# Kernel tuning notes

Hardware: AMD Instinct MI355X
Metric: run time of the kernel (lower is better)

## Reference

```python
import jax, jax.numpy as jnp
import numpy as np
import math

B, T, C, H, E = 1, 384, 512, 8, 16
D = C // H

def layer_norm(x, w, b, eps=1e-5):
    mu = jnp.mean(x, axis=-1, keepdims=True)
    var = jnp.mean(jnp.square(x - mu), axis=-1, keepdims=True)
    return (x - mu) * jax.lax.rsqrt(var + eps) * w + b

def setup_inputs() -> dict:
    key = jax.random.key(0)
    ks = jax.random.split(key, 12)
    s = 0.02
    return {
        'x': jax.random.normal(ks[0], (B, T, C), jnp.float32),
        'bias_matrix': jax.random.randint(ks[1], (B, T, T), 0, E, jnp.int32),
        'ln1_w': jnp.ones((C,), jnp.float32),
        'ln1_b': jnp.zeros((C,), jnp.float32),
        'w_attn_w': jax.random.normal(ks[2], (3 * C, C), jnp.float32) * s,
        'w_attn_b': jnp.zeros((3 * C,), jnp.float32),
        'w_proj_w': jax.random.normal(ks[3], (C, C), jnp.float32) * s,
        'w_proj_b': jnp.zeros((C,), jnp.float32),
        'attn_bias_emb': jax.random.normal(ks[4], (E, H), jnp.float32) * s,
        'edge_emb': jax.random.normal(ks[5], (E, C), jnp.float32) * s,
        'w_edge_k_w': jax.random.normal(ks[6], (C, C), jnp.float32) * s,
        'w_edge_k_b': jnp.zeros((C,), jnp.float32),
        'w_edge_v_w': jax.random.normal(ks[7], (C, C), jnp.float32) * s,
        'w_edge_v_b': jnp.zeros((C,), jnp.float32),
        'ln2_w': jnp.ones((C,), jnp.float32),
        'ln2_b': jnp.zeros((C,), jnp.float32),
        'c_fc_w': jax.random.normal(ks[8], (4 * C, C), jnp.float32) * s,
        'c_fc_b': jnp.zeros((4 * C,), jnp.float32),
        'c_proj_w': jax.random.normal(ks[9], (C, 4 * C), jnp.float32) * s,
        'c_proj_b': jnp.zeros((C,), jnp.float32),
    }

def reference(x, bias_matrix, ln1_w, ln1_b, w_attn_w, w_attn_b, w_proj_w, w_proj_b,
              attn_bias_emb, edge_emb, w_edge_k_w, w_edge_k_b, w_edge_v_w, w_edge_v_b,
              ln2_w, ln2_b, c_fc_w, c_fc_b, c_proj_w, c_proj_b):
    # --- attention branch ---
    h = layer_norm(x, ln1_w, ln1_b)
    qkv = h @ w_attn_w.T + w_attn_b                      # (B,T,3C)
    q, k, v = jnp.split(qkv, 3, axis=-1)
    q = q.reshape(B, T, H, D).transpose(0, 2, 1, 3)      # (B,H,T,D)
    k = k.reshape(B, T, H, D).transpose(0, 2, 1, 3)
    v = v.reshape(B, T, H, D).transpose(0, 2, 1, 3)
    scale = math.sqrt(D)

    ee = edge_emb[bias_matrix]                           # (B,T,T,C)
    e_k = (ee @ w_edge_k_w.T + w_edge_k_b).reshape(B, T, T, H, D)
    # score[b,h,i,j] = sum_d q[b,h,i,d] * k[b,h,j,d] * e_k[b,i,j,h,d]
    scores = jnp.einsum('bhid,bhjd,bijhd->bhij', q, k, e_k) / scale

    mask = jnp.tril(jnp.ones((T, T), bool))              # causal, diag included
    scores = jnp.where(mask, scores, -jnp.inf)
    ab = attn_bias_emb[bias_matrix].transpose(0, 3, 1, 2)  # (B,H,T,T)
    ab = jnp.where(mask, ab, 0.0)
    attn = jax.nn.softmax(scores + ab, axis=-1)

    e_v = (ee @ w_edge_v_w.T + w_edge_v_b).reshape(B, T, T, H, D)
    # y[b,h,i,d] = sum_j attn[b,h,i,j] * v[b,h,j,d] * e_v[b,i,j,h,d]
    y = jnp.einsum('bhij,bhjd,bijhd->bhid', attn, v, e_v)
    y = y.transpose(0, 2, 1, 3).reshape(B, T, C)
    y = y @ w_proj_w.T + w_proj_b
    x = x + y

    # --- MLP branch ---
    h2 = layer_norm(x, ln2_w, ln2_b)
    h2 = jax.nn.gelu(h2 @ c_fc_w.T + c_fc_b, approximate=False)
    x = x + (h2 @ c_proj_w.T + c_proj_b)
    return x
```

## Files before the change

kernel.cpp:

```cpp
#include <hip/hip_runtime.h>
#include <math.h>

#define TT 384
#define CC 512
#define HH 8
#define EE 16

typedef __bf16 bf16_t;
typedef __bf16 bf16x8 __attribute__((ext_vector_type(8)));
typedef __bf16 bf16x4v __attribute__((ext_vector_type(4)));
typedef float f32x4 __attribute__((ext_vector_type(4)));

__device__ __forceinline__ float wave_reduce_sum(float v) {
#pragma unroll
  for (int off = 32; off >= 1; off >>= 1) v += __shfl_xor(v, off, 64);
  return v;
}
__device__ __forceinline__ float wave_reduce_max(float v) {
#pragma unroll
  for (int off = 32; off >= 1; off >>= 1) v = fmaxf(v, __shfl_xor(v, off, 64));
  return v;
}

__global__ __launch_bounds__(256) void pre_k(
    const float* __restrict__ x, const float* __restrict__ ln1_w,
    const float* __restrict__ ln1_b, bf16_t* __restrict__ hbuf,
    const float* __restrict__ edge_emb, const float* __restrict__ wk,
    const float* __restrict__ kb, const float* __restrict__ wv,
    const float* __restrict__ vb, float* __restrict__ ek_tab,
    float* __restrict__ ev_tab) {
  __shared__ float sh[8];
  int tid = threadIdx.x;
  if (blockIdx.x < 384) {
    int row = blockIdx.x;
    const float* xr = x + (size_t)row * CC;
    float v0 = xr[tid], v1 = xr[tid + 256];
    float s = wave_reduce_sum(v0 + v1);
    float q = wave_reduce_sum(v0 * v0 + v1 * v1);
    int wv_ = tid >> 6, ln_ = tid & 63;
    if (ln_ == 0) { sh[wv_] = s; sh[4 + wv_] = q; }
    __syncthreads();
    float stot = sh[0] + sh[1] + sh[2] + sh[3];
    float qtot = sh[4] + sh[5] + sh[6] + sh[7];
    float mu = stot * (1.0f / 512.0f);
    float var = qtot * (1.0f / 512.0f) - mu * mu;
    float rs = rsqrtf(var + 1e-5f);
    hbuf[(size_t)row * CC + tid] =
        (bf16_t)((v0 - mu) * rs * ln1_w[tid] + ln1_b[tid]);
    hbuf[(size_t)row * CC + tid + 256] =
        (bf16_t)((v1 - mu) * rs * ln1_w[tid + 256] + ln1_b[tid + 256]);
  } else {
    int wid = (blockIdx.x - 384) * 4 + (tid >> 6);
    int lane = tid & 63;
    int gbase = wid * 16;
    int table = gbase >> 13;
    int e = (gbase >> 9) & 15;
    int c0 = gbase & 511;
    const float* er = edge_emb + e * 512 + lane * 8;
    f32x4 ea = *(const f32x4*)er;
    f32x4 eb = *(const f32x4*)(er + 4);
    const float* wbase = table ? wv : wk;
    const float* bbase = table ? vb : kb;
    float* obase = (table ? ev_tab : ek_tab) + e * 512;
#pragma unroll
    for (int o = 0; o < 16; o++) {
      int c = c0 + o;
      const float* wr = wbase + (size_t)c * 512 + lane * 8;
      f32x4 wa = *(const f32x4*)wr;
      f32x4 wb = *(const f32x4*)(wr + 4);
      float acc = ea.x * wa.x + ea.y * wa.y + ea.z * wa.z + ea.w * wa.w +
                  eb.x * wb.x + eb.y * wb.y + eb.z * wb.z + eb.w * wb.w;
      acc = wave_reduce_sum(acc);
      if (lane == 0) obase[c] = acc + bbase[c];
    }
  }
}

__global__ void ln_k(const float* __restrict__ xin, const float* __restrict__ w,
                     const float* __restrict__ b, bf16_t* __restrict__ out) {
  __shared__ float sh[8];
  int row = blockIdx.x, tid = threadIdx.x;
  const float* xr = xin + (size_t)row * CC;
  float v0 = xr[tid], v1 = xr[tid + 256];
  float s = wave_reduce_sum(v0 + v1);
  float q = wave_reduce_sum(v0 * v0 + v1 * v1);
  int wv_ = tid >> 6, ln_ = tid & 63;
  if (ln_ == 0) { sh[wv_] = s; sh[4 + wv_] = q; }
  __syncthreads();
  float stot = sh[0] + sh[1] + sh[2] + sh[3];
  float qtot = sh[4] + sh[5] + sh[6] + sh[7];
  float mu = stot * (1.0f / 512.0f);
  float var = qtot * (1.0f / 512.0f) - mu * mu;
  float rs = rsqrtf(var + 1e-5f);
  out[(size_t)row * CC + tid] = (bf16_t)((v0 - mu) * rs * w[tid] + b[tid]);
  out[(size_t)row * CC + tid + 256] =
      (bf16_t)((v1 - mu) * rs * w[tid + 256] + b[tid + 256]);
}

__device__ __forceinline__ bf16x8 load_w_frag(const float* p) {
  f32x4 a = *(const f32x4*)p;
  f32x4 b = *(const f32x4*)(p + 4);
  bf16x8 r;
  r[0] = (bf16_t)a.x; r[1] = (bf16_t)a.y; r[2] = (bf16_t)a.z; r[3] = (bf16_t)a.w;
  r[4] = (bf16_t)b.x; r[5] = (bf16_t)b.y; r[6] = (bf16_t)b.z; r[7] = (bf16_t)b.w;
  return r;
}

template <int MODE>
__global__ __launch_bounds__(256) void gemm_sk(
    const bf16_t* __restrict__ A, const float* __restrict__ W,
    const float* __restrict__ bias, const float* __restrict__ res,
    void* __restrict__ out, int N, int K) {
  __shared__ float part[4][32][32];
  int tid = threadIdx.x;
  int lane = tid & 63, wave = tid >> 6;
  int m0 = blockIdx.y * 32, n0 = blockIdx.x * 32;
  int r16 = lane & 15, quad = lane >> 4;
  int kchunk = K >> 2;
  int k0 = wave * kchunk;

  f32x4 acc[2][2];
  f32x4 zero = {0.f, 0.f, 0.f, 0.f};
#pragma unroll
  for (int i = 0; i < 2; i++)
#pragma unroll
    for (int j = 0; j < 2; j++) acc[i][j] = zero;

  const bf16_t* Ap = A + (size_t)(m0 + r16) * K + k0 + quad * 8;
  const float* Wp = W + (size_t)(n0 + r16) * K + k0 + quad * 8;
  for (int kb = 0; kb < kchunk; kb += 32) {
    bf16x8 af[2], bfr[2];
#pragma unroll
    for (int t = 0; t < 2; t++)
      af[t] = *(const bf16x8*)(Ap + (size_t)t * 16 * K + kb);
#pragma unroll
    for (int t = 0; t < 2; t++)
      bfr[t] = load_w_frag(Wp + (size_t)t * 16 * K + kb);
#pragma unroll
    for (int i = 0; i < 2; i++)
#pragma unroll
      for (int j = 0; j < 2; j++)
        acc[i][j] = __builtin_amdgcn_mfma_f32_16x16x32_bf16(af[i], bfr[j],
                                                            acc[i][j], 0, 0, 0);
  }

#pragma unroll
  for (int i = 0; i < 2; i++)
#pragma unroll
    for (int j = 0; j < 2; j++)
#pragma unroll
      for (int r = 0; r < 4; r++)
        part[wave][i * 16 + quad * 4 + r][j * 16 + r16] = acc[i][j][r];
  __syncthreads();

  int row = tid >> 3, c4 = (tid & 7) * 4;
  f32x4 v = *(const f32x4*)&part[0][row][c4];
  v += *(const f32x4*)&part[1][row][c4];
  v += *(const f32x4*)&part[2][row][c4];
  v += *(const f32x4*)&part[3][row][c4];
  int grow = m0 + row, gcol = n0 + c4;
  v += *(const f32x4*)(bias + gcol);
  if (MODE == 1) {
#pragma unroll
    for (int t = 0; t < 4; t++)
      v[t] = 0.5f * v[t] * (1.0f + erff(v[t] * 0.70710678118654752f));
  }
  if (MODE == 2 || MODE == 3) {
    v += *(const f32x4*)(res + (size_t)grow * N + gcol);
    *(f32x4*)((float*)out + (size_t)grow * N + gcol) = v;
  } else {
    bf16x4v o;
#pragma unroll
    for (int t = 0; t < 4; t++) o[t] = (bf16_t)v[t];
    *(bf16x4v*)((bf16_t*)out + (size_t)grow * N + gcol) = o;
  }
}

__global__ __launch_bounds__(256) void attn_k(
    const bf16_t* __restrict__ qkv, const int* __restrict__ bias_matrix,
    const float* __restrict__ attn_bias_emb, const float* __restrict__ ek_tab,
    const float* __restrict__ ev_tab, bf16_t* __restrict__ ybuf) {
  __shared__ float s[TT];
  __shared__ int ebuf[TT];
  __shared__ float qe[EE][68];
  __shared__ float evh[EE * 64];
  __shared__ float red[4 * 64];
  __shared__ float absh[EE];
  __shared__ float scr[8];

  int i = blockIdx.x, h = blockIdx.y;
  int tid = threadIdx.x, lane = tid & 63, wave = tid >> 6;
  int n = i + 1;

  for (int j = tid; j < n; j += 256) ebuf[j] = bias_matrix[i * TT + j];
  if (tid < EE) absh[tid] = attn_bias_emb[tid * HH + h];
  for (int idx = tid; idx < EE * 64; idx += 256) {
    int e = idx >> 6, d = idx & 63;
    float qv = (float)qkv[(size_t)i * 1536 + h * 64 + d];
    qe[e][d] = qv * ek_tab[e * 512 + h * 64 + d];
    evh[idx] = ev_tab[e * 512 + h * 64 + d];
  }
  __syncthreads();

  for (int jl = tid; jl < n; jl += 256) {
    int e = ebuf[jl];
    const uint4* kp = (const uint4*)(qkv + (size_t)jl * 1536 + 512 + h * 64);
    uint4 kr[8];
#pragma unroll
    for (int dg = 0; dg < 8; dg++) kr[dg] = kp[dg];
    float acc = 0.f;
#pragma unroll
    for (int dg = 0; dg < 8; dg++) {
      bf16x8 kv = *reinterpret_cast<const bf16x8*>(&kr[dg]);
      f32x4 qa = *(const f32x4*)&qe[e][dg * 8];
      f32x4 qb = *(const f32x4*)&qe[e][dg * 8 + 4];
      acc += (float)kv[0] * qa.x + (float)kv[1] * qa.y +
             (float)kv[2] * qa.z + (float)kv[3] * qa.w +
             (float)kv[4] * qb.x + (float)kv[5] * qb.y +
             (float)kv[6] * qb.z + (float)kv[7] * qb.w;
    }
    s[jl] = acc * 0.125f + absh[e];
  }
  __syncthreads();

  float lm = -1e30f;
  for (int j = tid; j < n; j += 256) lm = fmaxf(lm, s[j]);
  lm = wave_reduce_max(lm);
  if (lane == 0) scr[wave] = lm;
  __syncthreads();
  float mx = fmaxf(fmaxf(scr[0], scr[1]), fmaxf(scr[2], scr[3]));
  float ls = 0.0f;
  for (int j = tid; j < n; j += 256) {
    float p = __expf(s[j] - mx);
    s[j] = p;
    ls += p;
  }
  ls = wave_reduce_sum(ls);
  if (lane == 0) scr[4 + wave] = ls;
  __syncthreads();
  float inv = 1.0f / (scr[4] + scr[5] + scr[6] + scr[7]);

  float acc = 0.0f;
  int j = wave;
  for (; j + 4 < n; j += 8) {
    int e0 = ebuf[j], e1 = ebuf[j + 4];
    float p0 = s[j], p1 = s[j + 4];
    float v0 = (float)qkv[(size_t)j * 1536 + 1024 + h * 64 + lane];
    float v1 = (float)qkv[(size_t)(j + 4) * 1536 + 1024 + h * 64 + lane];
    acc += p0 * v0 * evh[e0 * 64 + lane] + p1 * v1 * evh[e1 * 64 + lane];
  }
  for (; j < n; j += 4) {
    int e = ebuf[j];
    float vv = (float)qkv[(size_t)j * 1536 + 1024 + h * 64 + lane];
    acc += s[j] * vv * evh[e * 64 + lane];
  }
  red[wave * 64 + lane] = acc;
  __syncthreads();
  if (tid < 64) {
    float y = (red[tid] + red[64 + tid] + red[128 + tid] + red[192 + tid]) * inv;
    ybuf[(size_t)i * CC + h * 64 + tid] = (bf16_t)y;
  }
}

extern "C" void kernel_launch(void* const* d_in, const int* in_sizes, int n_in,
                              void* d_out, int out_size, void* d_ws,
                              size_t ws_size, hipStream_t stream) {
  const float* x = (const float*)d_in[0];
  const int* bias_mat = (const int*)d_in[1];
  const float* ln1_w = (const float*)d_in[2];
  const float* ln1_b = (const float*)d_in[3];
  const float* w_attn_w = (const float*)d_in[4];
  const float* w_attn_b = (const float*)d_in[5];
  const float* w_proj_w = (const float*)d_in[6];
  const float* w_proj_b = (const float*)d_in[7];
  const float* attn_bias_emb = (const float*)d_in[8];
  const float* edge_emb = (const float*)d_in[9];
  const float* w_edge_k_w = (const float*)d_in[10];
  const float* w_edge_k_b = (const float*)d_in[11];
  const float* w_edge_v_w = (const float*)d_in[12];
  const float* w_edge_v_b = (const float*)d_in[13];
  const float* ln2_w = (const float*)d_in[14];
  const float* ln2_b = (const float*)d_in[15];
  const float* c_fc_w = (const float*)d_in[16];
  const float* c_fc_b = (const float*)d_in[17];
  const float* c_proj_w = (const float*)d_in[18];
  const float* c_proj_b = (const float*)d_in[19];

  char* wp = (char*)d_ws;
  float* ek_tab = (float*)wp;   wp += 16 * 512 * 4;
  float* ev_tab = (float*)wp;   wp += 16 * 512 * 4;
  bf16_t* hbuf = (bf16_t*)wp;   wp += 384 * 512 * 2;
  bf16_t* qkv = (bf16_t*)wp;    wp += 384 * 1536 * 2;
  bf16_t* ybuf = (bf16_t*)wp;   wp += 384 * 512 * 2;
  float* x1 = (float*)wp;       wp += 384 * 512 * 4;
  bf16_t* h2 = (bf16_t*)wp;     wp += 384 * 512 * 2;
  bf16_t* gbuf = (bf16_t*)wp;   wp += 384 * 2048 * 2;

  pre_k<<<640, 256, 0, stream>>>(x, ln1_w, ln1_b, hbuf, edge_emb, w_edge_k_w,
                                 w_edge_k_b, w_edge_v_w, w_edge_v_b, ek_tab,
                                 ev_tab);
  gemm_sk<0><<<dim3(48, 12), 256, 0, stream>>>(hbuf, w_attn_w, w_attn_b,
                                               nullptr, qkv, 1536, 512);
  attn_k<<<dim3(TT, HH), 256, 0, stream>>>(qkv, bias_mat, attn_bias_emb,
                                           ek_tab, ev_tab, ybuf);
  gemm_sk<2><<<dim3(16, 12), 256, 0, stream>>>(ybuf, w_proj_w, w_proj_b, x, x1,
                                               512, 512);
  ln_k<<<384, 256, 0, stream>>>(x1, ln2_w, ln2_b, h2);
  gemm_sk<1><<<dim3(64, 12), 256, 0, stream>>>(h2, c_fc_w, c_fc_b, nullptr,
                                               gbuf, 2048, 512);
  gemm_sk<3><<<dim3(16, 12), 256, 0, stream>>>(gbuf, c_proj_w, c_proj_b, x1,
                                               (float*)d_out, 512, 2048);
}
```

Baseline: 182.6 us.

## Fuse all stages into one persistent kernel with grid barriers

Replaces the seven kernel launches with one persistent kernel of 512 blocks. The stages are separated by atomic-counter grid barriers, and a shared-memory union is reused across stages. All weights are converted to bf16 once in the first phase, so the GEMM inner loops load bf16 directly. Attention work is paired as row p with row 383-p to balance the causal load. This is meant to remove launch gaps and the fp32-to-bf16 conversion in the GEMM loops, at the cost of spin-wait barriers, a memset launch and a deadlock risk if not all blocks are co-resident.

```diff
diff --git a/kernel.cpp b/kernel.cpp
--- a/kernel.cpp
+++ b/kernel.cpp
@@ -5,12 +5,31 @@
 #define CC 512
 #define HH 8
 #define EE 16
+#define GRID 512
 
 typedef __bf16 bf16_t;
 typedef __bf16 bf16x8 __attribute__((ext_vector_type(8)));
 typedef __bf16 bf16x4v __attribute__((ext_vector_type(4)));
 typedef float f32x4 __attribute__((ext_vector_type(4)));
 
+struct Args {
+  const float* x; const int* bm;
+  const float *ln1w, *ln1b, *wattnb, *wprojb, *abemb, *eemb;
+  const float *wekw, *wekb, *wevw, *wevb, *ln2w, *ln2b, *cfcb, *cprojb;
+  const float *wattn, *wproj, *cfcw, *cprojw;
+  float *ektab, *evtab, *x1, *out;
+  bf16_t *hbuf, *qkv, *ybuf, *h2, *gbuf;
+  bf16_t *wattn_bf, *wproj_bf, *cfc_bf, *cproj_bf;
+  unsigned* bar;
+};
+
+struct SharedG { float part[4][32][32]; };
+struct SharedA {
+  float s[TT]; int ebuf[TT]; float qe[EE][68]; float evh[EE * 64];
+  float red[256]; float absh[EE]; float scr[8];
+};
+union SharedU { SharedG g; SharedA a; float sh[8]; };
+
 __device__ __forceinline__ float wave_reduce_sum(float v) {
 #pragma unroll
   for (int off = 32; off >= 1; off >>= 1) v += __shfl_xor(v, off, 64);
@@ -22,73 +41,33 @@
   return v;
 }
 
-__global__ __launch_bounds__(256) void pre_k(
-    const float* __restrict__ x, const float* __restrict__ ln1_w,
-    const float* __restrict__ ln1_b, bf16_t* __restrict__ hbuf,
-    const float* __restrict__ edge_emb, const float* __restrict__ wk,
-    const float* __restrict__ kb, const float* __restrict__ wv,
-    const float* __restrict__ vb, float* __restrict__ ek_tab,
-    float* __restrict__ ev_tab) {
-  __shared__ float sh[8];
+__device__ __forceinline__ void gbar(unsigned* c) {
+  __syncthreads();
+  if (threadIdx.x == 0) {
+    __threadfence();
+    __hip_atomic_fetch_add(c, 1u, __ATOMIC_ACQ_REL, __HIP_MEMORY_SCOPE_AGENT);
+    while (__hip_atomic_load(c, __ATOMIC_ACQUIRE, __HIP_MEMORY_SCOPE_AGENT) <
+           (unsigned)GRID)
+      __builtin_amdgcn_s_sleep(2);
+    __threadfence();
+  }
+  __syncthreads();
+}
+
+__device__ void ln_row(const float* __restrict__ xin, const float* __restrict__ w,
+                       const float* __restrict__ b, bf16_t* __restrict__ out,
+                       int row, SharedU& su) {
   int tid = threadIdx.x;
-  if (blockIdx.x < 384) {
-    int row = blockIdx.x;
-    const float* xr = x + (size_t)row * CC;
-    float v0 = xr[tid], v1 = xr[tid + 256];
-    float s = wave_reduce_sum(v0 + v1);
-    float q = wave_reduce_sum(v0 * v0 + v1 * v1);
-    int wv_ = tid >> 6, ln_ = tid & 63;
-    if (ln_ == 0) { sh[wv_] = s; sh[4 + wv_] = q; }
-    __syncthreads();
-    float stot = sh[0] + sh[1] + sh[2] + sh[3];
-    float qtot = sh[4] + sh[5] + sh[6] + sh[7];
-    float mu = stot * (1.0f / 512.0f);
-    float var = qtot * (1.0f / 512.0f) - mu * mu;
-    float rs = rsqrtf(var + 1e-5f);
-    hbuf[(size_t)row * CC + tid] =
-        (bf16_t)((v0 - mu) * rs * ln1_w[tid] + ln1_b[tid]);
-    hbuf[(size_t)row * CC + tid + 256] =
-        (bf16_t)((v1 - mu) * rs * ln1_w[tid + 256] + ln1_b[tid + 256]);
-  } else {
-    int wid = (blockIdx.x - 384) * 4 + (tid >> 6);
-    int lane = tid & 63;
-    int gbase = wid * 16;
-    int table = gbase >> 13;
-    int e = (gbase >> 9) & 15;
-    int c0 = gbase & 511;
-    const float* er = edge_emb + e * 512 + lane * 8;
-    f32x4 ea = *(const f32x4*)er;
-    f32x4 eb = *(const f32x4*)(er + 4);
-    const float* wbase = table ? wv : wk;
-    const float* bbase = table ? vb : kb;
-    float* obase = (table ? ev_tab : ek_tab) + e * 512;
-#pragma unroll
-    for (int o = 0; o < 16; o++) {
-      int c = c0 + o;
-      const float* wr = wbase + (size_t)c * 512 + lane * 8;
-      f32x4 wa = *(const f32x4*)wr;
-      f32x4 wb = *(const f32x4*)(wr + 4);
-      float acc = ea.x * wa.x + ea.y * wa.y + ea.z * wa.z + ea.w * wa.w +
-                  eb.x * wb.x + eb.y * wb.y + eb.z * wb.z + eb.w * wb.w;
-      acc = wave_reduce_sum(acc);
-      if (lane == 0) obase[c] = acc + bbase[c];
-    }
-  }
-}
-
-__global__ void ln_k(const float* __restrict__ xin, const float* __restrict__ w,
-                     const float* __restrict__ b, bf16_t* __restrict__ out) {
-  __shared__ float sh[8];
-  int row = blockIdx.x, tid = threadIdx.x;
+  __syncthreads();
   const float* xr = xin + (size_t)row * CC;
   float v0 = xr[tid], v1 = xr[tid + 256];
   float s = wave_reduce_sum(v0 + v1);
   float q = wave_reduce_sum(v0 * v0 + v1 * v1);
   int wv_ = tid >> 6, ln_ = tid & 63;
-  if (ln_ == 0) { sh[wv_] = s; sh[4 + wv_] = q; }
-  __syncthreads();
-  float stot = sh[0] + sh[1] + sh[2] + sh[3];
-  float qtot = sh[4] + sh[5] + sh[6] + sh[7];
+  if (ln_ == 0) { su.sh[wv_] = s; su.sh[4 + wv_] = q; }
+  __syncthreads();
+  float stot = su.sh[0] + su.sh[1] + su.sh[2] + su.sh[3];
+  float qtot = su.sh[4] + su.sh[5] + su.sh[6] + su.sh[7];
   float mu = stot * (1.0f / 512.0f);
   float var = qtot * (1.0f / 512.0f) - mu * mu;
   float rs = rsqrtf(var + 1e-5f);
@@ -97,27 +76,41 @@
       (bf16_t)((v1 - mu) * rs * w[tid + 256] + b[tid + 256]);
 }
 
-__device__ __forceinline__ bf16x8 load_w_frag(const float* p) {
-  f32x4 a = *(const f32x4*)p;
-  f32x4 b = *(const f32x4*)(p + 4);
-  bf16x8 r;
-  r[0] = (bf16_t)a.x; r[1] = (bf16_t)a.y; r[2] = (bf16_t)a.z; r[3] = (bf16_t)a.w;
-  r[4] = (bf16_t)b.x; r[5] = (bf16_t)b.y; r[6] = (bf16_t)b.z; r[7] = (bf16_t)b.w;
-  return r;
+__device__ void table_unit(int idx, const Args& A) {
+  int tid = threadIdx.x, lane = tid & 63;
+  int wid = idx * 4 + (tid >> 6);
+  int gbase = wid * 16;
+  int table = gbase >> 13;
+  int e = (gbase >> 9) & 15;
+  int c0 = gbase & 511;
+  const float* er = A.eemb + e * 512 + lane * 8;
+  f32x4 ea = *(const f32x4*)er;
+  f32x4 eb = *(const f32x4*)(er + 4);
+  const float* wbase = table ? A.wevw : A.wekw;
+  const float* bbase = table ? A.wevb : A.wekb;
+  float* obase = (table ? A.evtab : A.ektab) + e * 512;
+#pragma unroll
+  for (int o = 0; o < 16; o++) {
+    int c = c0 + o;
+    const float* wr = wbase + (size_t)c * 512 + lane * 8;
+    f32x4 wa = *(const f32x4*)wr;
+    f32x4 wb = *(const f32x4*)(wr + 4);
+    float acc = ea.x * wa.x + ea.y * wa.y + ea.z * wa.z + ea.w * wa.w +
+                eb.x * wb.x + eb.y * wb.y + eb.z * wb.z + eb.w * wb.w;
+    acc = wave_reduce_sum(acc);
+    if (lane == 0) obase[c] = acc + bbase[c];
+  }
 }
 
 template <int MODE>
-__global__ __launch_bounds__(256) void gemm_sk(
-    const bf16_t* __restrict__ A, const float* __restrict__ W,
-    const float* __restrict__ bias, const float* __restrict__ res,
-    void* __restrict__ out, int N, int K) {
-  __shared__ float part[4][32][32];
-  int tid = threadIdx.x;
-  int lane = tid & 63, wave = tid >> 6;
-  int m0 = blockIdx.y * 32, n0 = blockIdx.x * 32;
+__device__ void gemm_tile(const bf16_t* __restrict__ Abase,
+                          const bf16_t* __restrict__ Wb,
+                          const float* __restrict__ bias,
+                          const float* __restrict__ res, void* __restrict__ out,
+                          int N, int K, int m0, int n0, SharedU& su) {
+  int tid = threadIdx.x, lane = tid & 63, wave = tid >> 6;
   int r16 = lane & 15, quad = lane >> 4;
-  int kchunk = K >> 2;
-  int k0 = wave * kchunk;
+  int kchunk = K >> 2, k0 = wave * kchunk;
 
   f32x4 acc[2][2];
   f32x4 zero = {0.f, 0.f, 0.f, 0.f};
@@ -126,8 +119,8 @@
 #pragma unroll
     for (int j = 0; j < 2; j++) acc[i][j] = zero;
 
-  const bf16_t* Ap = A + (size_t)(m0 + r16) * K + k0 + quad * 8;
-  const float* Wp = W + (size_t)(n0 + r16) * K + k0 + quad * 8;
+  const bf16_t* Ap = Abase + (size_t)(m0 + r16) * K + k0 + quad * 8;
+  const bf16_t* Wp = Wb + (size_t)(n0 + r16) * K + k0 + quad * 8;
   for (int kb = 0; kb < kchunk; kb += 32) {
     bf16x8 af[2], bfr[2];
 #pragma unroll
@@ -135,7 +128,7 @@
       af[t] = *(const bf16x8*)(Ap + (size_t)t * 16 * K + kb);
 #pragma unroll
     for (int t = 0; t < 2; t++)
-      bfr[t] = load_w_frag(Wp + (size_t)t * 16 * K + kb);
+      bfr[t] = *(const bf16x8*)(Wp + (size_t)t * 16 * K + kb);
 #pragma unroll
     for (int i = 0; i < 2; i++)
 #pragma unroll
@@ -144,20 +137,21 @@
                                                             acc[i][j], 0, 0, 0);
   }
 
+  __syncthreads();
 #pragma unroll
   for (int i = 0; i < 2; i++)
 #pragma unroll
     for (int j = 0; j < 2; j++)
 #pragma unroll
       for (int r = 0; r < 4; r++)
-        part[wave][i * 16 + quad * 4 + r][j * 16 + r16] = acc[i][j][r];
+        su.g.part[wave][i * 16 + quad * 4 + r][j * 16 + r16] = acc[i][j][r];
   __syncthreads();
 
   int row = tid >> 3, c4 = (tid & 7) * 4;
-  f32x4 v = *(const f32x4*)&part[0][row][c4];
-  v += *(const f32x4*)&part[1][row][c4];
-  v += *(const f32x4*)&part[2][row][c4];
-  v += *(const f32x4*)&part[3][row][c4];
+  f32x4 v = *(const f32x4*)&su.g.part[0][row][c4];
+  v += *(const f32x4*)&su.g.part[1][row][c4];
+  v += *(const f32x4*)&su.g.part[2][row][c4];
+  v += *(const f32x4*)&su.g.part[3][row][c4];
   int grow = m0 + row, gcol = n0 + c4;
   v += *(const f32x4*)(bias + gcol);
   if (MODE == 1) {
@@ -176,35 +170,25 @@
   }
 }
 
-__global__ __launch_bounds__(256) void attn_k(
-    const bf16_t* __restrict__ qkv, const int* __restrict__ bias_matrix,
-    const float* __restrict__ attn_bias_emb, const float* __restrict__ ek_tab,
-    const float* __restrict__ ev_tab, bf16_t* __restrict__ ybuf) {
-  __shared__ float s[TT];
-  __shared__ int ebuf[TT];
-  __shared__ float qe[EE][68];
-  __shared__ float evh[EE * 64];
-  __shared__ float red[4 * 64];
-  __shared__ float absh[EE];
-  __shared__ float scr[8];
-
-  int i = blockIdx.x, h = blockIdx.y;
+__device__ void attn_one(int i, int h, const Args& A, SharedU& su) {
+  SharedA& sa = su.a;
   int tid = threadIdx.x, lane = tid & 63, wave = tid >> 6;
   int n = i + 1;
-
-  for (int j = tid; j < n; j += 256) ebuf[j] = bias_matrix[i * TT + j];
-  if (tid < EE) absh[tid] = attn_bias_emb[tid * HH + h];
+  __syncthreads();
+
+  for (int j = tid; j < n; j += 256) sa.ebuf[j] = A.bm[i * TT + j];
+  if (tid < EE) sa.absh[tid] = A.abemb[tid * HH + h];
   for (int idx = tid; idx < EE * 64; idx += 256) {
     int e = idx >> 6, d = idx & 63;
-    float qv = (float)qkv[(size_t)i * 1536 + h * 64 + d];
-    qe[e][d] = qv * ek_tab[e * 512 + h * 64 + d];
-    evh[idx] = ev_tab[e * 512 + h * 64 + d];
+    float qv = (float)A.qkv[(size_t)i * 1536 + h * 64 + d];
+    sa.qe[e][d] = qv * A.ektab[e * 512 + h * 64 + d];
+    sa.evh[idx] = A.evtab[e * 512 + h * 64 + d];
   }
   __syncthreads();
 
   for (int jl = tid; jl < n; jl += 256) {
-    int e = ebuf[jl];
-    const uint4* kp = (const uint4*)(qkv + (size_t)jl * 1536 + 512 + h * 64);
+    int e = sa.ebuf[jl];
+    const uint4* kp = (const uint4*)(A.qkv + (size_t)jl * 1536 + 512 + h * 64);
     uint4 kr[8];
 #pragma unroll
     for (int dg = 0; dg < 8; dg++) kr[dg] = kp[dg];
@@ -212,102 +196,152 @@
 #pragma unroll
     for (int dg = 0; dg < 8; dg++) {
       bf16x8 kv = *reinterpret_cast<const bf16x8*>(&kr[dg]);
-      f32x4 qa = *(const f32x4*)&qe[e][dg * 8];
-      f32x4 qb = *(const f32x4*)&qe[e][dg * 8 + 4];
-      acc += (float)kv[0] * qa.x + (float)kv[1] * qa.y +
-             (float)kv[2] * qa.z + (float)kv[3] * qa.w +
-             (float)kv[4] * qb.x + (float)kv[5] * qb.y +
+      f32x4 qa = *(const f32x4*)&sa.qe[e][dg * 8];
+      f32x4 qb = *(const f32x4*)&sa.qe[e][dg * 8 + 4];
+      acc += (float)kv[0] * qa.x + (float)kv[1] * qa.y + (float)kv[2] * qa.z +
+             (float)kv[3] * qa.w + (float)kv[4] * qb.x + (float)kv[5] * qb.y +
              (float)kv[6] * qb.z + (float)kv[7] * qb.w;
     }
-    s[jl] = acc * 0.125f + absh[e];
+    sa.s[jl] = acc * 0.125f + sa.absh[e];
   }
   __syncthreads();
 
   float lm = -1e30f;
-  for (int j = tid; j < n; j += 256) lm = fmaxf(lm, s[j]);
+  for (int j = tid; j < n; j += 256) lm = fmaxf(lm, sa.s[j]);
   lm = wave_reduce_max(lm);
-  if (lane == 0) scr[wave] = lm;
-  __syncthreads();
-  float mx = fmaxf(fmaxf(scr[0], scr[1]), fmaxf(scr[2], scr[3]));
+  if (lane == 0) sa.scr[wave] = lm;
+  __syncthreads();
+  float mx = fmaxf(fmaxf(sa.scr[0], sa.scr[1]), fmaxf(sa.scr[2], sa.scr[3]));
   float ls = 0.0f;
   for (int j = tid; j < n; j += 256) {
-    float p = __expf(s[j] - mx);
-    s[j] = p;
+    float p = __expf(sa.s[j] - mx);
+    sa.s[j] = p;
     ls += p;
   }
   ls = wave_reduce_sum(ls);
-  if (lane == 0) scr[4 + wave] = ls;
-  __syncthreads();
-  float inv = 1.0f / (scr[4] + scr[5] + scr[6] + scr[7]);
+  if (lane == 0) sa.scr[4 + wave] = ls;
+  __syncthreads();
+  float inv = 1.0f / (sa.scr[4] + sa.scr[5] + sa.scr[6] + sa.scr[7]);
 
   float acc = 0.0f;
   int j = wave;
   for (; j + 4 < n; j += 8) {
-    int e0 = ebuf[j], e1 = ebuf[j + 4];
-    float p0 = s[j], p1 = s[j + 4];
-    float v0 = (float)qkv[(size_t)j * 1536 + 1024 + h * 64 + lane];
-    float v1 = (float)qkv[(size_t)(j + 4) * 1536 + 1024 + h * 64 + lane];
-    acc += p0 * v0 * evh[e0 * 64 + lane] + p1 * v1 * evh[e1 * 64 + lane];
+    int e0 = sa.ebuf[j], e1 = sa.ebuf[j + 4];
+    float p0 = sa.s[j], p1 = sa.s[j + 4];
+    float v0 = (float)A.qkv[(size_t)j * 1536 + 1024 + h * 64 + lane];
+    float v1 = (float)A.qkv[(size_t)(j + 4) * 1536 + 1024 + h * 64 + lane];
+    acc += p0 * v0 * sa.evh[e0 * 64 + lane] + p1 * v1 * sa.evh[e1 * 64 + lane];
   }
   for (; j < n; j += 4) {
-    int e = ebuf[j];
-    float vv = (float)qkv[(size_t)j * 1536 + 1024 + h * 64 + lane];
-    acc += s[j] * vv * evh[e * 64 + lane];
-  }
-  red[wave * 64 + lane] = acc;
+    int e = sa.ebuf[j];
+    float vv = (float)A.qkv[(size_t)j * 1536 + 1024 + h * 64 + lane];
+    acc += sa.s[j] * vv * sa.evh[e * 64 + lane];
+  }
+  sa.red[wave * 64 + lane] = acc;
   __syncthreads();
   if (tid < 64) {
-    float y = (red[tid] + red[64 + tid] + red[128 + tid] + red[192 + tid]) * inv;
-    ybuf[(size_t)i * CC + h * 64 + tid] = (bf16_t)y;
-  }
+    float y = (sa.red[tid] + sa.red[64 + tid] + sa.red[128 + tid] +
+               sa.red[192 + tid]) * inv;
+    A.ybuf[(size_t)i * CC + h * 64 + tid] = (bf16_t)y;
+  }
+}
+
+__global__ __launch_bounds__(256, 2) void fused_k(Args A) {
+  __shared__ SharedU su;
+  int bid = blockIdx.x, tid = threadIdx.x;
+
+  for (int u = bid; u < 640; u += GRID) {
+    if (u < 256) table_unit(u, A);
+    else ln_row(A.x, A.ln1w, A.ln1b, A.hbuf, u - 256, su);
+  }
+  {
+    int g = bid * 256 + tid;
+    for (int v = g; v < 786432; v += GRID * 256) {
+      const float* src; bf16_t* dst; int loc;
+      if (v < 196608)      { src = A.wattn;  dst = A.wattn_bf; loc = v; }
+      else if (v < 262144) { src = A.wproj;  dst = A.wproj_bf; loc = v - 196608; }
+      else if (v < 524288) { src = A.cfcw;   dst = A.cfc_bf;   loc = v - 262144; }
+      else                 { src = A.cprojw; dst = A.cproj_bf; loc = v - 524288; }
+      f32x4 a = *((const f32x4*)src + loc);
+      bf16x4v o;
+      o[0] = (bf16_t)a.x; o[1] = (bf16_t)a.y; o[2] = (bf16_t)a.z; o[3] = (bf16_t)a.w;
+      *((bf16x4v*)dst + loc) = o;
+    }
+  }
+  gbar(A.bar + 0);
+
+  for (int u = bid; u < 576; u += GRID)
+    gemm_tile<0>(A.hbuf, A.wattn_bf, A.wattnb, nullptr, A.qkv, 1536, 512,
+                 (u / 48) * 32, (u % 48) * 32, su);
+  gbar(A.bar + 1);
+
+  for (int u = bid; u < 1536; u += GRID) {
+    int p = u >> 3, h = u & 7;
+    attn_one(p, h, A, su);
+    attn_one(383 - p, h, A, su);
+  }
+  gbar(A.bar + 2);
+
+  for (int u = bid; u < 192; u += GRID)
+    gemm_tile<2>(A.ybuf, A.wproj_bf, A.wprojb, A.x, A.x1, 512, 512,
+                 (u / 16) * 32, (u % 16) * 32, su);
+  gbar(A.bar + 3);
+
+  for (int u = bid; u < 384; u += GRID)
+    ln_row(A.x1, A.ln2w, A.ln2b, A.h2, u, su);
+  gbar(A.bar + 4);
+
+  for (int u = bid; u < 768; u += GRID)
+    gemm_tile<1>(A.h2, A.cfc_bf, A.cfcb, nullptr, A.gbuf, 2048, 512,
+                 (u / 64) * 32, (u % 64) * 32, su);
+  gbar(A.bar + 5);
+
+  for (int u = bid; u < 192; u += GRID)
+    gemm_tile<3>(A.gbuf, A.cproj_bf, A.cprojb, A.x1, A.out, 512, 2048,
+                 (u / 16) * 32, (u % 16) * 32, su);
 }
 
 extern "C" void kernel_launch(void* const* d_in, const int* in_sizes, int n_in,
                               void* d_out, int out_size, void* d_ws,
                               size_t ws_size, hipStream_t stream) {
-  const float* x = (const float*)d_in[0];
-  const int* bias_mat = (const int*)d_in[1];
-  const float* ln1_w = (const float*)d_in[2];
-  const float* ln1_b = (const float*)d_in[3];
-  const float* w_attn_w = (const float*)d_in[4];
-  const float* w_attn_b = (const float*)d_in[5];
-  const float* w_proj_w = (const float*)d_in[6];
-  const float* w_proj_b = (const float*)d_in[7];
-  const float* attn_bias_emb = (const float*)d_in[8];
-  const float* edge_emb = (const float*)d_in[9];
-  const float* w_edge_k_w = (const float*)d_in[10];
-  const float* w_edge_k_b = (const float*)d_in[11];
-  const float* w_edge_v_w = (const float*)d_in[12];
-  const float* w_edge_v_b = (const float*)d_in[13];
-  const float* ln2_w = (const float*)d_in[14];
-  const float* ln2_b = (const float*)d_in[15];
-  const float* c_fc_w = (const float*)d_in[16];
-  const float* c_fc_b = (const float*)d_in[17];
-  const float* c_proj_w = (const float*)d_in[18];
-  const float* c_proj_b = (const float*)d_in[19];
+  Args A;
+  A.x = (const float*)d_in[0];
+  A.bm = (const int*)d_in[1];
+  A.ln1w = (const float*)d_in[2];
+  A.ln1b = (const float*)d_in[3];
+  A.wattn = (const float*)d_in[4];
+  A.wattnb = (const float*)d_in[5];
+  A.wproj = (const float*)d_in[6];
+  A.wprojb = (const float*)d_in[7];
+  A.abemb = (const float*)d_in[8];
+  A.eemb = (const float*)d_in[9];
+  A.wekw = (const float*)d_in[10];
+  A.wekb = (const float*)d_in[11];
+  A.wevw = (const float*)d_in[12];
+  A.wevb = (const float*)d_in[13];
+  A.ln2w = (const float*)d_in[14];
+  A.ln2b = (const float*)d_in[15];
+  A.cfcw = (const float*)d_in[16];
+  A.cfcb = (const float*)d_in[17];
+  A.cprojw = (const float*)d_in[18];
+  A.cprojb = (const float*)d_in[19];
+  A.out = (float*)d_out;
 
   char* wp = (char*)d_ws;
-  float* ek_tab = (float*)wp;   wp += 16 * 512 * 4;
-  float* ev_tab = (float*)wp;   wp += 16 * 512 * 4;
-  bf16_t* hbuf = (bf16_t*)wp;   wp += 384 * 512 * 2;
-  bf16_t* qkv = (bf16_t*)wp;    wp += 384 * 1536 * 2;
-  bf16_t* ybuf = (bf16_t*)wp;   wp += 384 * 512 * 2;
-  float* x1 = (float*)wp;       wp += 384 * 512 * 4;
-  bf16_t* h2 = (bf16_t*)wp;     wp += 384 * 512 * 2;
-  bf16_t* gbuf = (bf16_t*)wp;   wp += 384 * 2048 * 2;
-
-  pre_k<<<640, 256, 0, stream>>>(x, ln1_w, ln1_b, hbuf, edge_emb, w_edge_k_w,
-                                 w_edge_k_b, w_edge_v_w, w_edge_v_b, ek_tab,
-                                 ev_tab);
-  gemm_sk<0><<<dim3(48, 12), 256, 0, stream>>>(hbuf, w_attn_w, w_attn_b,
-                                               nullptr, qkv, 1536, 512);
-  attn_k<<<dim3(TT, HH), 256, 0, stream>>>(qkv, bias_mat, attn_bias_emb,
-                                           ek_tab, ev_tab, ybuf);
-  gemm_sk<2><<<dim3(16, 12), 256, 0, stream>>>(ybuf, w_proj_w, w_proj_b, x, x1,
-                                               512, 512);
-  ln_k<<<384, 256, 0, stream>>>(x1, ln2_w, ln2_b, h2);
-  gemm_sk<1><<<dim3(64, 12), 256, 0, stream>>>(h2, c_fc_w, c_fc_b, nullptr,
-                                               gbuf, 2048, 512);
-  gemm_sk<3><<<dim3(16, 12), 256, 0, stream>>>(gbuf, c_proj_w, c_proj_b, x1,
-                                               (float*)d_out, 512, 2048);
-}
+  A.ektab = (float*)wp;    wp += 16 * 512 * 4;
+  A.evtab = (float*)wp;    wp += 16 * 512 * 4;
+  A.x1 = (float*)wp;       wp += 384 * 512 * 4;
+  A.hbuf = (bf16_t*)wp;    wp += 384 * 512 * 2;
+  A.qkv = (bf16_t*)wp;     wp += 384 * 1536 * 2;
+  A.ybuf = (bf16_t*)wp;    wp += 384 * 512 * 2;
+  A.h2 = (bf16_t*)wp;      wp += 384 * 512 * 2;
+  A.gbuf = (bf16_t*)wp;    wp += 384 * 2048 * 2;
+  A.wattn_bf = (bf16_t*)wp; wp += 1536 * 512 * 2;
+  A.wproj_bf = (bf16_t*)wp; wp += 512 * 512 * 2;
+  A.cfc_bf = (bf16_t*)wp;   wp += 2048 * 512 * 2;
+  A.cproj_bf = (bf16_t*)wp; wp += 512 * 2048 * 2;
+  A.bar = (unsigned*)wp;    wp += 64;
+
+  hipMemsetAsync(A.bar, 0, 64, stream);
+  fused_k<<<GRID, 256, 0, stream>>>(A);
+}
```

After: 645.6 us. 3.54x slower.

## Fold layernorms into GEMM epilogues and pre-convert weights to bf16

Applied to the files above, without the earlier changes.

Both layer norms are folded algebraically into the following GEMMs. The prologue precomputes gamma-scaled bf16 weight rows plus per-column sums and bias constants, and each GEMM applies the row mean and rstd in its epilogue. LN2 row statistics are accumulated with atomics in the projection GEMM's epilogue, so the separate ln_k kernel and the normalized activation buffers go away. All four weight matrices are converted to bf16 once per call in the prologue, so GEMM inner loops load bf16 weights directly instead of converting fp32 on the fly. The trade-offs are extra prologue work, atomics, one-pass variance, and some precision risk from casting unnormalized activations to bf16 before the mean is subtracted.

```diff
diff --git a/kernel.cpp b/kernel.cpp
--- a/kernel.cpp
+++ b/kernel.cpp
@@ -22,46 +22,50 @@
   return v;
 }
 
-__global__ __launch_bounds__(256) void pre_k(
-    const float* __restrict__ x, const float* __restrict__ ln1_w,
-    const float* __restrict__ ln1_b, bf16_t* __restrict__ hbuf,
-    const float* __restrict__ edge_emb, const float* __restrict__ wk,
-    const float* __restrict__ kb, const float* __restrict__ wv,
-    const float* __restrict__ vb, float* __restrict__ ek_tab,
-    float* __restrict__ ev_tab) {
-  __shared__ float sh[8];
-  int tid = threadIdx.x;
-  if (blockIdx.x < 384) {
-    int row = blockIdx.x;
-    const float* xr = x + (size_t)row * CC;
-    float v0 = xr[tid], v1 = xr[tid + 256];
-    float s = wave_reduce_sum(v0 + v1);
-    float q = wave_reduce_sum(v0 * v0 + v1 * v1);
-    int wv_ = tid >> 6, ln_ = tid & 63;
-    if (ln_ == 0) { sh[wv_] = s; sh[4 + wv_] = q; }
-    __syncthreads();
-    float stot = sh[0] + sh[1] + sh[2] + sh[3];
-    float qtot = sh[4] + sh[5] + sh[6] + sh[7];
-    float mu = stot * (1.0f / 512.0f);
-    float var = qtot * (1.0f / 512.0f) - mu * mu;
-    float rs = rsqrtf(var + 1e-5f);
-    hbuf[(size_t)row * CC + tid] =
-        (bf16_t)((v0 - mu) * rs * ln1_w[tid] + ln1_b[tid]);
-    hbuf[(size_t)row * CC + tid + 256] =
-        (bf16_t)((v1 - mu) * rs * ln1_w[tid + 256] + ln1_b[tid + 256]);
-  } else {
-    int wid = (blockIdx.x - 384) * 4 + (tid >> 6);
-    int lane = tid & 63;
+struct PreArgs {
+  const float *x, *ln1w, *ln1b, *wattn, *wattnb, *eemb, *wekw, *wekb, *wevw,
+      *wevb, *ln2w, *ln2b, *cfcw, *cfcb, *wproj, *wcproj;
+  float *ektab, *evtab, *xmu, *xrs, *x1s1, *x1s2, *s1q, *cq, *s1f, *cf;
+  bf16_t *wqkv_bf, *wfc_bf, *wproj_bf, *wcproj_bf;
+};
+
+__device__ __forceinline__ void wrow_unit(const float* __restrict__ wr,
+                                          const float* __restrict__ g,
+                                          const float* __restrict__ bb,
+                                          float extra_c, bf16_t* __restrict__ orow,
+                                          float* __restrict__ s1p,
+                                          float* __restrict__ cp, int lane) {
+  const float* p = wr + lane * 8;
+  f32x4 w0 = *(const f32x4*)p, w1 = *(const f32x4*)(p + 4);
+  f32x4 g0 = *(const f32x4*)(g + lane * 8), g1 = *(const f32x4*)(g + lane * 8 + 4);
+  f32x4 b0 = *(const f32x4*)(bb + lane * 8), b1 = *(const f32x4*)(bb + lane * 8 + 4);
+  f32x4 p0 = w0 * g0, p1 = w1 * g1;
+  bf16x8 o;
+  o[0] = (bf16_t)p0.x; o[1] = (bf16_t)p0.y; o[2] = (bf16_t)p0.z; o[3] = (bf16_t)p0.w;
+  o[4] = (bf16_t)p1.x; o[5] = (bf16_t)p1.y; o[6] = (bf16_t)p1.z; o[7] = (bf16_t)p1.w;
+  *(bf16x8*)(orow + lane * 8) = o;
+  float s1 = p0.x + p0.y + p0.z + p0.w + p1.x + p1.y + p1.z + p1.w;
+  float c = w0.x * b0.x + w0.y * b0.y + w0.z * b0.z + w0.w * b0.w +
+            w1.x * b1.x + w1.y * b1.y + w1.z * b1.z + w1.w * b1.w;
+  s1 = wave_reduce_sum(s1);
+  c = wave_reduce_sum(c);
+  if (lane == 0) { *s1p = s1; *cp = c + extra_c; }
+}
+
+__global__ __launch_bounds__(256) void pre_k(PreArgs P) {
+  int b = blockIdx.x, tid = threadIdx.x, lane = tid & 63, wave = tid >> 6;
+  if (b < 256) {
+    int wid = b * 4 + wave;
     int gbase = wid * 16;
     int table = gbase >> 13;
     int e = (gbase >> 9) & 15;
     int c0 = gbase & 511;
-    const float* er = edge_emb + e * 512 + lane * 8;
+    const float* er = P.eemb + e * 512 + lane * 8;
     f32x4 ea = *(const f32x4*)er;
     f32x4 eb = *(const f32x4*)(er + 4);
-    const float* wbase = table ? wv : wk;
-    const float* bbase = table ? vb : kb;
-    float* obase = (table ? ev_tab : ek_tab) + e * 512;
+    const float* wbase = table ? P.wevw : P.wekw;
+    const float* bbase = table ? P.wevb : P.wekb;
+    float* obase = (table ? P.evtab : P.ektab) + e * 512;
 #pragma unroll
     for (int o = 0; o < 16; o++) {
       int c = c0 + o;
@@ -73,51 +77,63 @@
       acc = wave_reduce_sum(acc);
       if (lane == 0) obase[c] = acc + bbase[c];
     }
-  }
-}
-
-__global__ void ln_k(const float* __restrict__ xin, const float* __restrict__ w,
-                     const float* __restrict__ b, bf16_t* __restrict__ out) {
-  __shared__ float sh[8];
-  int row = blockIdx.x, tid = threadIdx.x;
-  const float* xr = xin + (size_t)row * CC;
-  float v0 = xr[tid], v1 = xr[tid + 256];
-  float s = wave_reduce_sum(v0 + v1);
-  float q = wave_reduce_sum(v0 * v0 + v1 * v1);
-  int wv_ = tid >> 6, ln_ = tid & 63;
-  if (ln_ == 0) { sh[wv_] = s; sh[4 + wv_] = q; }
-  __syncthreads();
-  float stot = sh[0] + sh[1] + sh[2] + sh[3];
-  float qtot = sh[4] + sh[5] + sh[6] + sh[7];
-  float mu = stot * (1.0f / 512.0f);
-  float var = qtot * (1.0f / 512.0f) - mu * mu;
-  float rs = rsqrtf(var + 1e-5f);
-  out[(size_t)row * CC + tid] = (bf16_t)((v0 - mu) * rs * w[tid] + b[tid]);
-  out[(size_t)row * CC + tid + 256] =
-      (bf16_t)((v1 - mu) * rs * w[tid + 256] + b[tid + 256]);
-}
-
-__device__ __forceinline__ bf16x8 load_w_frag(const float* p) {
-  f32x4 a = *(const f32x4*)p;
-  f32x4 b = *(const f32x4*)(p + 4);
-  bf16x8 r;
-  r[0] = (bf16_t)a.x; r[1] = (bf16_t)a.y; r[2] = (bf16_t)a.z; r[3] = (bf16_t)a.w;
-  r[4] = (bf16_t)b.x; r[5] = (bf16_t)b.y; r[6] = (bf16_t)b.z; r[7] = (bf16_t)b.w;
-  return r;
+  } else if (b < 640) {
+    int n = (b - 256) * 4 + wave;
+    wrow_unit(P.wattn + (size_t)n * 512, P.ln1w, P.ln1b, P.wattnb[n],
+              P.wqkv_bf + (size_t)n * 512, P.s1q + n, P.cq + n, lane);
+  } else if (b < 1152) {
+    int n = (b - 640) * 4 + wave;
+    wrow_unit(P.cfcw + (size_t)n * 512, P.ln2w, P.ln2b, P.cfcb[n],
+              P.wfc_bf + (size_t)n * 512, P.s1f + n, P.cf + n, lane);
+  } else if (b < 1216) {
+    int base = (b - 1152) * 1024;
+    for (int u = tid; u < 1024; u += 256) {
+      f32x4 a = *((const f32x4*)P.wproj + base + u);
+      bf16x4v o;
+      o[0] = (bf16_t)a.x; o[1] = (bf16_t)a.y; o[2] = (bf16_t)a.z; o[3] = (bf16_t)a.w;
+      *((bf16x4v*)P.wproj_bf + base + u) = o;
+    }
+  } else if (b < 1472) {
+    int base = (b - 1216) * 1024;
+    for (int u = tid; u < 1024; u += 256) {
+      f32x4 a = *((const f32x4*)P.wcproj + base + u);
+      bf16x4v o;
+      o[0] = (bf16_t)a.x; o[1] = (bf16_t)a.y; o[2] = (bf16_t)a.z; o[3] = (bf16_t)a.w;
+      *((bf16x4v*)P.wcproj_bf + base + u) = o;
+    }
+  } else if (b < 1568) {
+    int r = (b - 1472) * 4 + wave;
+    const float* xr = P.x + (size_t)r * 512 + lane * 8;
+    f32x4 a = *(const f32x4*)xr, c = *(const f32x4*)(xr + 4);
+    float s = a.x + a.y + a.z + a.w + c.x + c.y + c.z + c.w;
+    float q = a.x * a.x + a.y * a.y + a.z * a.z + a.w * a.w +
+              c.x * c.x + c.y * c.y + c.z * c.z + c.w * c.w;
+    s = wave_reduce_sum(s);
+    q = wave_reduce_sum(q);
+    if (lane == 0) {
+      float mu = s * (1.0f / 512.0f);
+      float var = q * (1.0f / 512.0f) - mu * mu;
+      P.xmu[r] = mu;
+      P.xrs[r] = rsqrtf(var + 1e-5f);
+    }
+  } else {
+    for (int i = tid; i < 384; i += 256) { P.x1s1[i] = 0.f; P.x1s2[i] = 0.f; }
+  }
 }
 
 template <int MODE>
-__global__ __launch_bounds__(256) void gemm_sk(
-    const bf16_t* __restrict__ A, const float* __restrict__ W,
-    const float* __restrict__ bias, const float* __restrict__ res,
-    void* __restrict__ out, int N, int K) {
+__global__ __launch_bounds__(256) void gemm_k(
+    const void* __restrict__ Aptr, const bf16_t* __restrict__ Wb,
+    const float* __restrict__ e0, const float* __restrict__ e1,
+    const float* __restrict__ e2, const float* __restrict__ e3,
+    const float* __restrict__ res, void* __restrict__ out,
+    float* __restrict__ st1, float* __restrict__ st2, int N, int K) {
+  constexpr bool AF32 = (MODE == 0 || MODE == 2);
   __shared__ float part[4][32][32];
-  int tid = threadIdx.x;
-  int lane = tid & 63, wave = tid >> 6;
+  int tid = threadIdx.x, lane = tid & 63, wave = tid >> 6;
   int m0 = blockIdx.y * 32, n0 = blockIdx.x * 32;
   int r16 = lane & 15, quad = lane >> 4;
-  int kchunk = K >> 2;
-  int k0 = wave * kchunk;
+  int kchunk = K >> 2, k0 = wave * kchunk;
 
   f32x4 acc[2][2];
   f32x4 zero = {0.f, 0.f, 0.f, 0.f};
@@ -126,16 +142,27 @@
 #pragma unroll
     for (int j = 0; j < 2; j++) acc[i][j] = zero;
 
-  const bf16_t* Ap = A + (size_t)(m0 + r16) * K + k0 + quad * 8;
-  const float* Wp = W + (size_t)(n0 + r16) * K + k0 + quad * 8;
+  const float* Af = (const float*)Aptr + (size_t)(m0 + r16) * K + k0 + quad * 8;
+  const bf16_t* Ab = (const bf16_t*)Aptr + (size_t)(m0 + r16) * K + k0 + quad * 8;
+  const bf16_t* Wp = Wb + (size_t)(n0 + r16) * K + k0 + quad * 8;
   for (int kb = 0; kb < kchunk; kb += 32) {
     bf16x8 af[2], bfr[2];
 #pragma unroll
+    for (int t = 0; t < 2; t++) {
+      if (AF32) {
+        f32x4 a = *(const f32x4*)(Af + (size_t)t * 16 * K + kb);
+        f32x4 c = *(const f32x4*)(Af + (size_t)t * 16 * K + kb + 4);
+        af[t][0] = (bf16_t)a.x; af[t][1] = (bf16_t)a.y;
+        af[t][2] = (bf16_t)a.z; af[t][3] = (bf16_t)a.w;
+        af[t][4] = (bf16_t)c.x; af[t][5] = (bf16_t)c.y;
+        af[t][6] = (bf16_t)c.z; af[t][7] = (bf16_t)c.w;
+      } else {
+        af[t] = *(const bf16x8*)(Ab + (size_t)t * 16 * K + kb);
+      }
+    }
+#pragma unroll
     for (int t = 0; t < 2; t++)
-      af[t] = *(const bf16x8*)(Ap + (size_t)t * 16 * K + kb);
-#pragma unroll
-    for (int t = 0; t < 2; t++)
-      bfr[t] = load_w_frag(Wp + (size_t)t * 16 * K + kb);
+      bfr[t] = *(const bf16x8*)(Wp + (size_t)t * 16 * K + kb);
 #pragma unroll
     for (int i = 0; i < 2; i++)
 #pragma unroll
@@ -159,20 +186,44 @@
   v += *(const f32x4*)&part[2][row][c4];
   v += *(const f32x4*)&part[3][row][c4];
   int grow = m0 + row, gcol = n0 + c4;
-  v += *(const f32x4*)(bias + gcol);
-  if (MODE == 1) {
-#pragma unroll
-    for (int t = 0; t < 4; t++)
-      v[t] = 0.5f * v[t] * (1.0f + erff(v[t] * 0.70710678118654752f));
-  }
-  if (MODE == 2 || MODE == 3) {
+
+  if (MODE == 0 || MODE == 2) {
+    float mu, rs;
+    if (MODE == 0) {
+      mu = e0[grow]; rs = e1[grow];
+    } else {
+      float S = e0[grow], Q = e1[grow];
+      mu = S * (1.0f / 512.0f);
+      float var = Q * (1.0f / 512.0f) - mu * mu;
+      rs = rsqrtf(var + 1e-5f);
+    }
+    f32x4 s1v = *(const f32x4*)(e2 + gcol);
+    f32x4 ccv = *(const f32x4*)(e3 + gcol);
+#pragma unroll
+    for (int t = 0; t < 4; t++) {
+      float x = rs * (v[t] - mu * s1v[t]) + ccv[t];
+      if (MODE == 2) x = 0.5f * x * (1.0f + erff(x * 0.70710678118654752f));
+      v[t] = x;
+    }
+    bf16x4v o;
+#pragma unroll
+    for (int t = 0; t < 4; t++) o[t] = (bf16_t)v[t];
+    *(bf16x4v*)((bf16_t*)out + (size_t)grow * N + gcol) = o;
+  } else {
+    v += *(const f32x4*)(e2 + gcol);
     v += *(const f32x4*)(res + (size_t)grow * N + gcol);
     *(f32x4*)((float*)out + (size_t)grow * N + gcol) = v;
-  } else {
-    bf16x4v o;
-#pragma unroll
-    for (int t = 0; t < 4; t++) o[t] = (bf16_t)v[t];
-    *(bf16x4v*)((bf16_t*)out + (size_t)grow * N + gcol) = o;
+    if (MODE == 1) {
+      float sv = v.x + v.y + v.z + v.w;
+      float qv = v.x * v.x + v.y * v.y + v.z * v.z + v.w * v.w;
+      sv += __shfl_down(sv, 4, 8); qv += __shfl_down(qv, 4, 8);
+      sv += __shfl_down(sv, 2, 8); qv += __shfl_down(qv, 2, 8);
+      sv += __shfl_down(sv, 1, 8); qv += __shfl_down(qv, 1, 8);
+      if ((tid & 7) == 0) {
+        atomicAdd(st1 + grow, sv);
+        atomicAdd(st2 + grow, qv);
+      }
+    }
   }
 }
 
@@ -214,9 +265,8 @@
       bf16x8 kv = *reinterpret_cast<const bf16x8*>(&kr[dg]);
       f32x4 qa = *(const f32x4*)&qe[e][dg * 8];
       f32x4 qb = *(const f32x4*)&qe[e][dg * 8 + 4];
-      acc += (float)kv[0] * qa.x + (float)kv[1] * qa.y +
-             (float)kv[2] * qa.z + (float)kv[3] * qa.w +
-             (float)kv[4] * qb.x + (float)kv[5] * qb.y +
+      acc += (float)kv[0] * qa.x + (float)kv[1] * qa.y + (float)kv[2] * qa.z +
+             (float)kv[3] * qa.w + (float)kv[4] * qb.x + (float)kv[5] * qb.y +
              (float)kv[6] * qb.z + (float)kv[7] * qb.w;
     }
     s[jl] = acc * 0.125f + absh[e];
@@ -267,47 +317,63 @@
                               size_t ws_size, hipStream_t stream) {
   const float* x = (const float*)d_in[0];
   const int* bias_mat = (const int*)d_in[1];
-  const float* ln1_w = (const float*)d_in[2];
-  const float* ln1_b = (const float*)d_in[3];
-  const float* w_attn_w = (const float*)d_in[4];
-  const float* w_attn_b = (const float*)d_in[5];
-  const float* w_proj_w = (const float*)d_in[6];
-  const float* w_proj_b = (const float*)d_in[7];
-  const float* attn_bias_emb = (const float*)d_in[8];
-  const float* edge_emb = (const float*)d_in[9];
-  const float* w_edge_k_w = (const float*)d_in[10];
-  const float* w_edge_k_b = (const float*)d_in[11];
-  const float* w_edge_v_w = (const float*)d_in[12];
-  const float* w_edge_v_b = (const float*)d_in[13];
-  const float* ln2_w = (const float*)d_in[14];
-  const float* ln2_b = (const float*)d_in[15];
-  const float* c_fc_w = (const float*)d_in[16];
-  const float* c_fc_b = (const float*)d_in[17];
-  const float* c_proj_w = (const float*)d_in[18];
-  const float* c_proj_b = (const float*)d_in[19];
 
   char* wp = (char*)d_ws;
-  float* ek_tab = (float*)wp;   wp += 16 * 512 * 4;
-  float* ev_tab = (float*)wp;   wp += 16 * 512 * 4;
-  bf16_t* hbuf = (bf16_t*)wp;   wp += 384 * 512 * 2;
-  bf16_t* qkv = (bf16_t*)wp;    wp += 384 * 1536 * 2;
-  bf16_t* ybuf = (bf16_t*)wp;   wp += 384 * 512 * 2;
-  float* x1 = (float*)wp;       wp += 384 * 512 * 4;
-  bf16_t* h2 = (bf16_t*)wp;     wp += 384 * 512 * 2;
-  bf16_t* gbuf = (bf16_t*)wp;   wp += 384 * 2048 * 2;
-
-  pre_k<<<640, 256, 0, stream>>>(x, ln1_w, ln1_b, hbuf, edge_emb, w_edge_k_w,
-                                 w_edge_k_b, w_edge_v_w, w_edge_v_b, ek_tab,
-                                 ev_tab);
-  gemm_sk<0><<<dim3(48, 12), 256, 0, stream>>>(hbuf, w_attn_w, w_attn_b,
-                                               nullptr, qkv, 1536, 512);
-  attn_k<<<dim3(TT, HH), 256, 0, stream>>>(qkv, bias_mat, attn_bias_emb,
-                                           ek_tab, ev_tab, ybuf);
-  gemm_sk<2><<<dim3(16, 12), 256, 0, stream>>>(ybuf, w_proj_w, w_proj_b, x, x1,
-                                               512, 512);
-  ln_k<<<384, 256, 0, stream>>>(x1, ln2_w, ln2_b, h2);
-  gemm_sk<1><<<dim3(64, 12), 256, 0, stream>>>(h2, c_fc_w, c_fc_b, nullptr,
-                                               gbuf, 2048, 512);
-  gemm_sk<3><<<dim3(16, 12), 256, 0, stream>>>(gbuf, c_proj_w, c_proj_b, x1,
-                                               (float*)d_out, 512, 2048);
-}
+  float* ektab = (float*)wp;  wp += 16 * 512 * 4;
+  float* evtab = (float*)wp;  wp += 16 * 512 * 4;
+  float* xmu = (float*)wp;    wp += 384 * 4;
+  float* xrs = (float*)wp;    wp += 384 * 4;
+  float* x1s1 = (float*)wp;   wp += 384 * 4;
+  float* x1s2 = (float*)wp;   wp += 384 * 4;
+  float* s1q = (float*)wp;    wp += 1536 * 4;
+  float* cq = (float*)wp;     wp += 1536 * 4;
+  float* s1f = (float*)wp;    wp += 2048 * 4;
+  float* cf = (float*)wp;     wp += 2048 * 4;
+  float* x1 = (float*)wp;     wp += 384 * 512 * 4;
+  bf16_t* wqkv_bf = (bf16_t*)wp;   wp += 1536 * 512 * 2;
+  bf16_t* wfc_bf = (bf16_t*)wp;    wp += 2048 * 512 * 2;
+  bf16_t* wproj_bf = (bf16_t*)wp;  wp += 512 * 512 * 2;
+  bf16_t* wcproj_bf = (bf16_t*)wp; wp += 512 * 2048 * 2;
+  bf16_t* qkv = (bf16_t*)wp;  wp += 384 * 1536 * 2;
+  bf16_t* ybuf = (bf16_t*)wp; wp += 384 * 512 * 2;
+  bf16_t* gbuf = (bf16_t*)wp; wp += 384 * 2048 * 2;
+
+  PreArgs P;
+  P.x = x;
+  P.ln1w = (const float*)d_in[2];
+  P.ln1b = (const float*)d_in[3];
+  P.wattn = (const float*)d_in[4];
+  P.wattnb = (const float*)d_in[5];
+  P.eemb = (const float*)d_in[9];
+  P.wekw = (const float*)d_in[10];
+  P.wekb = (const float*)d_in[11];
+  P.wevw = (const float*)d_in[12];
+  P.wevb = (const float*)d_in[13];
+  P.ln2w = (const float*)d_in[14];
+  P.ln2b = (const float*)d_in[15];
+  P.cfcw = (const float*)d_in[16];
+  P.cfcb = (const float*)d_in[17];
+  P.wproj = (const float*)d_in[6];
+  P.wcproj = (const float*)d_in[18];
+  P.ektab = ektab; P.evtab = evtab; P.xmu = xmu; P.xrs = xrs;
+  P.x1s1 = x1s1; P.x1s2 = x1s2; P.s1q = s1q; P.cq = cq; P.s1f = s1f; P.cf = cf;
+  P.wqkv_bf = wqkv_bf; P.wfc_bf = wfc_bf; P.wproj_bf = wproj_bf;
+  P.wcproj_bf = wcproj_bf;
+
+  pre_k<<<1569, 256, 0, stream>>>(P);
+  gemm_k<0><<<dim3(48, 12), 256, 0, stream>>>(x, wqkv_bf, xmu, xrs, s1q, cq,
+                                              nullptr, qkv, nullptr, nullptr,
+                                              1536, 512);
+  attn_k<<<dim3(TT, HH), 256, 0, stream>>>(qkv, bias_mat,
+                                           (const float*)d_in[8], ektab, evtab,
+                                           ybuf);
+  gemm_k<1><<<dim3(16, 12), 256, 0, stream>>>(
+      ybuf, wproj_bf, nullptr, nullptr, (const float*)d_in[7], nullptr, x, x1,
+      x1s1, x1s2, 512, 512);
+  gemm_k<2><<<dim3(64, 12), 256, 0, stream>>>(x1, wfc_bf, x1s1, x1s2, s1f, cf,
+                                              nullptr, gbuf, nullptr, nullptr,
+                                              2048, 512);
+  gemm_k<3><<<dim3(16, 12), 256, 0, stream>>>(
+      gbuf, wcproj_bf, nullptr, nullptr, (const float*)d_in[19], nullptr, x1,
+      d_out, nullptr, nullptr, 512, 2048);
+}
```

Measured after the change: 177.0 us. 1.03x faster.
